# Optimization experiments

Hardware: AMD Instinct MI355X
Metric: run time of the kernel (lower is better)

The kernel has to match this reference:

```python
import jax, jax.numpy as jnp
import numpy as np

N_HEAD = 8
N_EMBD = 768
T_MAX = 1024


def setup_inputs() -> dict:
    key = jax.random.key(0)
    ks = jax.random.split(key, 5)
    B, T, C = 8, 1024, N_EMBD
    x = jax.random.normal(ks[0], (B, T, C), dtype=jnp.float32)
    c_attn_weight = jax.random.normal(ks[1], (3 * C, C), dtype=jnp.float32) * (1.0 / np.sqrt(C))
    c_attn_bias = jax.random.normal(ks[2], (3 * C,), dtype=jnp.float32) * 0.02
    c_proj_weight = jax.random.normal(ks[3], (C, C), dtype=jnp.float32) * (1.0 / np.sqrt(C))
    c_proj_bias = jax.random.normal(ks[4], (C,), dtype=jnp.float32) * 0.02
    bias = jnp.tril(jnp.ones((T_MAX, T_MAX), dtype=jnp.int32))[None, None]  # (1,1,Tmax,Tmax)
    return {
        "x": x,
        "c_attn_weight": c_attn_weight,
        "c_attn_bias": c_attn_bias,
        "c_proj_weight": c_proj_weight,
        "c_proj_bias": c_proj_bias,
        "bias": bias,
    }


def reference(x, c_attn_weight, c_attn_bias, c_proj_weight, c_proj_bias, bias):
    B, T, C = x.shape
    H = N_HEAD
    D = C // H  # head dim
    qkv = jnp.einsum("btc,fc->btf", x, c_attn_weight) + c_attn_bias  # (B,T,3C)
    q, k, v = jnp.split(qkv, 3, axis=-1)
    q = q.reshape(B, T, H, D).transpose(0, 2, 1, 3)  # (B,H,T,D)
    k = k.reshape(B, T, H, D).transpose(0, 2, 1, 3)
    v = v.reshape(B, T, H, D).transpose(0, 2, 1, 3)
    att = jnp.einsum("bhqd,bhkd->bhqk", q, k) * (1.0 / np.sqrt(D))  # (B,H,T,T)
    mask = bias[:, :, :T, :T] == 0
    att = jnp.where(mask, jnp.float32(-jnp.inf), att)
    att = jax.nn.softmax(att, axis=-1)
    y = jnp.einsum("bhqk,bhkd->bhqd", att, v)  # (B,H,T,D)
    y = y.transpose(0, 2, 1, 3).reshape(B, T, C)
    y = jnp.einsum("btc,fc->btf", y, c_proj_weight) + c_proj_bias
    return y
```

## Files before the change

### kernel.cpp

```cpp
#include <hip/hip_runtime.h>
#include <hip/hip_bf16.h>
#include <stdint.h>


typedef unsigned short ushort_t;
typedef __attribute__((ext_vector_type(8))) short short8;
typedef __attribute__((ext_vector_type(4))) float floatx4;
typedef __attribute__((ext_vector_type(4))) unsigned short ushort4v;

#define MFMA16(a, b, c) __builtin_amdgcn_mfma_f32_16x16x32_bf16(a, b, c, 0, 0, 0)
#define NEG_BIG (-1e30f)

__device__ __forceinline__ unsigned short f2bf(float f) {
  union { float f; unsigned int u; } v; v.f = f;
  unsigned int r = (v.u + 0x7FFFu + ((v.u >> 16) & 1u)) >> 16;
  return (unsigned short)r;
}

__device__ __forceinline__ unsigned int packbf2(float a, float b) {
  union { __hip_bfloat162 h; unsigned int u; } cv;
  cv.h = __float22bfloat162_rn(make_float2(a, b));
  return cv.u;
}

#define GLOAD16(src, dst)                                              \
  __builtin_amdgcn_global_load_lds(                                    \
      (const __attribute__((address_space(1))) void*)(src),            \
      (__attribute__((address_space(3))) void*)(dst), 16, 0, 0)

#define WAITBAR(VM)                                                    \
  do {                                                                 \
    asm volatile("s_waitcnt vmcnt(" #VM ")" ::: "memory");             \
    __builtin_amdgcn_s_barrier();                                      \
  } while (0)

#define WAITBAR_LGKM(VM)                                               \
  do {                                                                 \
    asm volatile("s_waitcnt vmcnt(" #VM ") lgkmcnt(0)" ::: "memory");  \
    __builtin_amdgcn_s_barrier();                                      \
  } while (0)

__global__ __launch_bounds__(256) void cvt3(
    const float* __restrict__ x, const float* __restrict__ wa,
    const float* __restrict__ wp, ushort_t* __restrict__ xb,
    ushort_t* __restrict__ wab, ushort_t* __restrict__ wpb)
{
  const int n1 = (8192 * 768) / 4, n2 = (2304 * 768) / 4;
  int i = blockIdx.x * 256 + threadIdx.x;
  const float* in; ushort_t* out;
  if (i < n1)            { in = x;  out = xb; }
  else if (i < n1 + n2)  { in = wa; out = wab; i -= n1; }
  else                   { in = wp; out = wpb; i -= (n1 + n2); }
  float4 v = *(const float4*)(in + (size_t)i * 4);
  ushort4v o;
  o.x = f2bf(v.x); o.y = f2bf(v.y); o.z = f2bf(v.z); o.w = f2bf(v.w);
  *(ushort4v*)(out + (size_t)i * 4) = o;
}

#define GEMM_STAGE(BUF, OFF)                                           \
  do {                                                                 \
    ushort_t* lA = &As[BUF][wid * 512];                                \
    ushort_t* lB = &Bs[BUF][wid * 512];                                \
    const ushort_t* pA = gA + (OFF);                                   \
    const ushort_t* pB = gB + (OFF);                                   \
    GLOAD16(pA, lA);                                                   \
    GLOAD16(pA + (size_t)64 * 768, lA + 64 * 32);                      \
    GLOAD16(pB, lB);                                                   \
    GLOAD16(pB + (size_t)64 * 768, lB + 64 * 32);                      \
  } while (0)

#define GEMM_COMPUTE(BUF)                                              \
  do {                                                                 \
    short8 af[4], bf[4];                                               \
    _Pragma("unroll")                                                  \
    for (int t_ = 0; t_ < 4; ++t_) {                                   \
      af[t_] = *(const short8*)&As[BUF][(wm + t_ * 16 + l15) * 32 + sw]; \
      bf[t_] = *(const short8*)&Bs[BUF][(wn + t_ * 16 + l15) * 32 + sw]; \
    }                                                                  \
    __builtin_amdgcn_s_setprio(1);                                     \
    _Pragma("unroll")                                                  \
    for (int tm = 0; tm < 4; ++tm)                                     \
      _Pragma("unroll")                                                \
      for (int tn = 0; tn < 4; ++tn)                                   \
        acc[tm][tn] = MFMA16(af[tm], bf[tn], acc[tm][tn]);             \
    __builtin_amdgcn_s_setprio(0);                                     \
  } while (0)

#define GEMM_KLOOP                                                     \
  do {                                                                 \
    GEMM_STAGE(0, 0);                                                  \
    GEMM_STAGE(1, 32);                                                 \
    _Pragma("unroll")                                                  \
    for (int t = 0; t < 24; ++t) {                                     \
      if (t < 23) WAITBAR(4); else WAITBAR(0);                         \
      if (t + 2 < 24) GEMM_STAGE((t + 2) % 3, (t + 2) * 32);           \
      GEMM_COMPUTE(t % 3);                                             \
    }                                                                  \
  } while (0)

__global__ __launch_bounds__(256) void gemm_qkv(
    const ushort_t* __restrict__ A,
    const ushort_t* __restrict__ W,
    const float* __restrict__ bias,
    ushort_t* __restrict__ QK,
    ushort_t* __restrict__ VT)
{
  const int K = 768;
  __shared__ ushort_t As[3][128 * 32];
  __shared__ ushort_t Bs[3][128 * 32];

  const int tid  = threadIdx.x;
  const int lane = tid & 63;
  const int l15  = lane & 15;
  const int quad = lane >> 4;
  const int wid  = tid >> 6;
  const int m0 = blockIdx.x * 128;
  const int n0 = blockIdx.y * 128;
  const int wm = (wid >> 1) * 64;
  const int wn = (wid & 1) * 64;
  const int srow = tid >> 2;
  const int scol = (((tid & 3) ^ ((srow ^ (srow >> 2)) & 3))) * 8;
  const int sw = (quad ^ ((l15 ^ (l15 >> 2)) & 3)) * 8;

  floatx4 acc[4][4] = {};

  const ushort_t* gA = A + (size_t)(m0 + srow) * K + scol;
  const ushort_t* gB = W + (size_t)(n0 + srow) * K + scol;

  GEMM_KLOOP;

  const float QSCALE = 0.10206207261596577f * 1.4426950408889634f;

#pragma unroll
  for (int tn = 0; tn < 4; ++tn) {
    const int gc = n0 + wn + tn * 16 + l15;
    const float bv = bias[gc];
    const bool isv = (gc >= 1536);
    const bool isq = (gc < 768);
    const int hh = (gc - 1536) / 96, dd = (gc - 1536) % 96;
#pragma unroll
    for (int tm = 0; tm < 4; ++tm) {
      const int gr = m0 + wm + tm * 16 + quad * 4;
#pragma unroll
      for (int r = 0; r < 4; ++r) {
        float val = acc[tm][tn][r] + bv;
        const int row = gr + r;
        if (!isv) {
          if (isq) val *= QSCALE;
          QK[(size_t)row * 1536 + gc] = f2bf(val);
        } else {
          const int bb = row >> 10, tt = row & 1023;
          const int tt2 = (tt & ~0x1C) | (((tt >> 4) & 1) << 2) |
                          (((tt >> 2) & 3) << 3);
          VT[(((size_t)(bb * 8 + hh)) * 96 + dd) * 1024 + tt2] = f2bf(val);
        }
      }
    }
  }
}

__global__ __launch_bounds__(256) void gemm_proj(
    const ushort_t* __restrict__ A,
    const ushort_t* __restrict__ W,
    const float* __restrict__ bias,
    float* __restrict__ C,
    int M, int N)
{
  const int K = 768;
  __shared__ ushort_t As[3][128 * 32];
  __shared__ ushort_t Bs[3][128 * 32];

  const int tid  = threadIdx.x;
  const int lane = tid & 63;
  const int l15  = lane & 15;
  const int quad = lane >> 4;
  const int wid  = tid >> 6;
  const int m0 = blockIdx.x * 128;
  const int n0 = blockIdx.y * 128;
  const int wm = (wid >> 1) * 64;
  const int wn = (wid & 1) * 64;
  const int srow = tid >> 2;
  const int scol = (((tid & 3) ^ ((srow ^ (srow >> 2)) & 3))) * 8;
  const int sw = (quad ^ ((l15 ^ (l15 >> 2)) & 3)) * 8;

  floatx4 acc[4][4] = {};

  const ushort_t* gA = A + (size_t)(m0 + srow) * K + scol;
  const ushort_t* gB = W + (size_t)(n0 + srow) * K + scol;

  GEMM_KLOOP;

#pragma unroll
  for (int tn = 0; tn < 4; ++tn) {
    const int gc = n0 + wn + tn * 16 + l15;
    const float bv = bias[gc];
#pragma unroll
    for (int tm = 0; tm < 4; ++tm) {
      const int gr = m0 + wm + tm * 16 + quad * 4;
#pragma unroll
      for (int r = 0; r < 4; ++r)
        C[(size_t)(gr + r) * N + gc] = acc[tm][tn][r] + bv;
    }
  }
}

__global__ __launch_bounds__(256) void attn_fused(
    const ushort_t* __restrict__ QK,
    const ushort_t* __restrict__ VT,
    ushort_t* __restrict__ y)
{
  __shared__ ushort_t Ks[2][64 * 96];
  __shared__ ushort_t Vt[2][96 * 72];

  const int tid  = threadIdx.x;
  const int lane = tid & 63;
  const int l15  = lane & 15;
  const int quad = lane >> 4;
  const int wid  = tid >> 6;
  const int bh = blockIdx.y;
  const int b = bh >> 3;
  const int h = bh & 7;
  const int qoff = h * 96;

  const int cA = blockIdx.x;
  const int cB = 31 - cA;
  const int myChunk = (wid < 2) ? cA : cB;
  const int q0w = myChunk * 32 + (wid & 1) * 16;
  const int kend = cB * 32 + 32;
  const int rq = q0w + l15;

  const size_t rowbase = (size_t)b * 1024;
  const ushort_t* vtb = VT + (size_t)bh * 96 * 1024;

  const int ke0 = wid * 1536 + lane * 8;
  const int vd  = (tid >> 3);
  const int vkc = (tid & 7) * 8;

  short8 qf[3];
#pragma unroll
  for (int c = 0; c < 3; ++c)
    qf[c] = *(const short8*)(QK + (rowbase + q0w + l15) * 1536 + qoff +
                             c * 32 + quad * 8);

  float m_i = NEG_BIG;
  float l_i = 0.f;
  floatx4 O[6] = {};

  short8 vreg[3];

#pragma unroll
  for (int g = 0; g < 3; ++g)
    vreg[g] = *(const short8*)(vtb + (size_t)(g * 32 + vd) * 1024 + vkc);
#pragma unroll
  for (int i = 0; i < 3; ++i) {
    const int e = ke0 + i * 512;
    const int kr = e / 96, kc = e % 96;
    GLOAD16(QK + (rowbase + kr) * 1536 + 768 + qoff + kc,
            &Ks[0][wid * 1536 + i * 512]);
  }
#pragma unroll
  for (int g = 0; g < 3; ++g)
    *(short8*)&Vt[0][(g * 32 + vd) * 72 + vkc] = vreg[g];
#pragma unroll
  for (int g = 0; g < 3; ++g)
    vreg[g] = *(const short8*)(vtb + (size_t)(g * 32 + vd) * 1024 + 64 + vkc);

  int cur = 0;
  for (int k0 = 0; k0 < kend; k0 += 64) {
    const int nk = k0 + 64;
    const bool more = (nk < kend);

    if (more) WAITBAR_LGKM(3); else WAITBAR_LGKM(0);

    if (more) {
#pragma unroll
      for (int i = 0; i < 3; ++i) {
        const int e = ke0 + i * 512;
        const int kr = e / 96, kc = e % 96;
        GLOAD16(QK + (rowbase + nk + kr) * 1536 + 768 + qoff + kc,
                &Ks[cur ^ 1][wid * 1536 + i * 512]);
      }
    }

    if (k0 < q0w + 16) {
      floatx4 s[4] = {};
      __builtin_amdgcn_s_setprio(1);
#pragma unroll
      for (int t = 0; t < 4; ++t) {
#pragma unroll
        for (int c = 0; c < 3; ++c) {
          short8 kf = *(const short8*)
              &Ks[cur][(t * 16 + l15) * 96 + c * 32 + quad * 8];
          s[t] = MFMA16(kf, qf[c], s[t]);
        }
      }
      __builtin_amdgcn_s_setprio(0);
      float p[4][4];
      if (k0 + 64 <= q0w) {
#pragma unroll
        for (int t = 0; t < 4; ++t)
#pragma unroll
          for (int j = 0; j < 4; ++j) p[t][j] = s[t][j];
      } else {
        const int kq = k0 + quad * 4;
#pragma unroll
        for (int t = 0; t < 4; ++t)
#pragma unroll
          for (int j = 0; j < 4; ++j)
            p[t][j] = (kq + t * 16 + j <= rq) ? s[t][j] : NEG_BIG;
      }
      float m0v = fmaxf(fmaxf(p[0][0], p[0][1]), fmaxf(p[0][2], p[0][3]));
      float m1v = fmaxf(fmaxf(p[1][0], p[1][1]), fmaxf(p[1][2], p[1][3]));
      float m2v = fmaxf(fmaxf(p[2][0], p[2][1]), fmaxf(p[2][2], p[2][3]));
      float m3v = fmaxf(fmaxf(p[3][0], p[3][1]), fmaxf(p[3][2], p[3][3]));
      float mt = fmaxf(fmaxf(m0v, m1v), fmaxf(m2v, m3v));
      mt = fmaxf(mt, __shfl_xor(mt, 16));
      mt = fmaxf(mt, __shfl_xor(mt, 32));
      if (!__all(mt - m_i <= 8.0f)) {
        const float mn = fmaxf(m_i, mt);
        const float al = __builtin_amdgcn_exp2f(m_i - mn);
        m_i = mn;
        l_i *= al;
#pragma unroll
        for (int j = 0; j < 4; ++j) {
          const float alr = __shfl(al, quad * 4 + j);
#pragma unroll
          for (int f = 0; f < 6; ++f) O[f][j] *= alr;
        }
      }
      float rs = 0.f;
#pragma unroll
      for (int t = 0; t < 4; ++t)
#pragma unroll
        for (int j = 0; j < 4; ++j) {
          p[t][j] = __builtin_amdgcn_exp2f(p[t][j] - m_i);
          rs += p[t][j];
        }
      rs += __shfl_xor(rs, 16);
      rs += __shfl_xor(rs, 32);
      l_i += rs;
      union { short8 s8; unsigned int u[4]; } pf0, pf1;
      pf0.u[0] = packbf2(p[0][0], p[0][1]);
      pf0.u[1] = packbf2(p[0][2], p[0][3]);
      pf0.u[2] = packbf2(p[1][0], p[1][1]);
      pf0.u[3] = packbf2(p[1][2], p[1][3]);
      pf1.u[0] = packbf2(p[2][0], p[2][1]);
      pf1.u[1] = packbf2(p[2][2], p[2][3]);
      pf1.u[2] = packbf2(p[3][0], p[3][1]);
      pf1.u[3] = packbf2(p[3][2], p[3][3]);
      __builtin_amdgcn_s_setprio(1);
#pragma unroll
      for (int f = 0; f < 6; ++f) {
        short8 vf0 = *(const short8*)&Vt[cur][(f * 16 + l15) * 72 + quad * 8];
        O[f] = MFMA16(pf0.s8, vf0, O[f]);
        short8 vf1 = *(const short8*)
            &Vt[cur][(f * 16 + l15) * 72 + 32 + quad * 8];
        O[f] = MFMA16(pf1.s8, vf1, O[f]);
      }
      __builtin_amdgcn_s_setprio(0);
    }

    if (more) {
#pragma unroll
      for (int g = 0; g < 3; ++g)
        *(short8*)&Vt[cur ^ 1][(g * 32 + vd) * 72 + vkc] = vreg[g];
      if (nk + 64 < kend) {
#pragma unroll
        for (int g = 0; g < 3; ++g)
          vreg[g] = *(const short8*)
              (vtb + (size_t)(g * 32 + vd) * 1024 + nk + 64 + vkc);
      }
    }
    cur ^= 1;
  }

  float inv[4];
#pragma unroll
  for (int j = 0; j < 4; ++j) {
    const float lj = __shfl(l_i, quad * 4 + j);
    inv[j] = 1.0f / fmaxf(lj, 1e-20f);
  }
#pragma unroll
  for (int j = 0; j < 4; ++j) {
    const size_t row = rowbase + q0w + quad * 4 + j;
#pragma unroll
    for (int f = 0; f < 6; ++f)
      y[row * 768 + qoff + f * 16 + l15] = f2bf(O[f][j] * inv[j]);
  }
}

extern "C" void kernel_launch(void* const* d_in, const int* in_sizes, int n_in,
                              void* d_out, int out_size, void* d_ws, size_t ws_size,
                              hipStream_t stream)
{
  const float* x_f  = (const float*)d_in[0];
  const float* wa_f = (const float*)d_in[1];
  const float* ba_f = (const float*)d_in[2];
  const float* wp_f = (const float*)d_in[3];
  const float* bp_f = (const float*)d_in[4];
  float* out = (float*)d_out;

  ushort_t* xb  = (ushort_t*)d_ws;
  ushort_t* wab = xb  + (size_t)8192 * 768;
  ushort_t* wpb = wab + (size_t)2304 * 768;
  ushort_t* QK  = wpb + (size_t)768 * 768;
  ushort_t* VT  = QK  + (size_t)8192 * 1536;
  ushort_t* yw  = VT  + (size_t)8192 * 768;

  cvt3<<<8448, 256, 0, stream>>>(x_f, wa_f, wp_f, xb, wab, wpb);

  gemm_qkv<<<dim3(64, 18), 256, 0, stream>>>(xb, wab, ba_f, QK, VT);
  attn_fused<<<dim3(16, 64), 256, 0, stream>>>(QK, VT, yw);
  gemm_proj<<<dim3(64, 6), 256, 0, stream>>>(yw, wpb, bp_f, out,
                                             8192, 768);
}
```

Before: 220.6 us.

## Drop LDS staging; use single-wave blocks loading operands directly from global

Both GEMMs and the attention kernel are rewritten to use single-wavefront blocks that load MFMA operands straight from global memory into registers, with register-level triple buffering in the GEMMs. This removes LDS tiles, barriers and async global-to-LDS copies. Attention drops the paired-chunk load balancing in favour of one 16-row query tile per block. The trade-off is a loss of data reuse across waves, so global/L2 traffic goes up, V reads become strided, and small blocks may load-balance poorly across the causal triangle.

```diff
diff --git a/kernel.cpp b/kernel.cpp
--- a/kernel.cpp
+++ b/kernel.cpp
@@ -22,23 +22,6 @@
   cv.h = __float22bfloat162_rn(make_float2(a, b));
   return cv.u;
 }
-
-#define GLOAD16(src, dst)                                              \
-  __builtin_amdgcn_global_load_lds(                                    \
-      (const __attribute__((address_space(1))) void*)(src),            \
-      (__attribute__((address_space(3))) void*)(dst), 16, 0, 0)
-
-#define WAITBAR(VM)                                                    \
-  do {                                                                 \
-    asm volatile("s_waitcnt vmcnt(" #VM ")" ::: "memory");             \
-    __builtin_amdgcn_s_barrier();                                      \
-  } while (0)
-
-#define WAITBAR_LGKM(VM)                                               \
-  do {                                                                 \
-    asm volatile("s_waitcnt vmcnt(" #VM ") lgkmcnt(0)" ::: "memory");  \
-    __builtin_amdgcn_s_barrier();                                      \
-  } while (0)
 
 __global__ __launch_bounds__(256) void cvt3(
     const float* __restrict__ x, const float* __restrict__ wa,
@@ -57,90 +40,74 @@
   *(ushort4v*)(out + (size_t)i * 4) = o;
 }
 
-#define GEMM_STAGE(BUF, OFF)                                           \
+#define SLD(AA, BB, KO)                                                \
   do {                                                                 \
-    ushort_t* lA = &As[BUF][wid * 512];                                \
-    ushort_t* lB = &Bs[BUF][wid * 512];                                \
-    const ushort_t* pA = gA + (OFF);                                   \
-    const ushort_t* pB = gB + (OFF);                                   \
-    GLOAD16(pA, lA);                                                   \
-    GLOAD16(pA + (size_t)64 * 768, lA + 64 * 32);                      \
-    GLOAD16(pB, lB);                                                   \
-    GLOAD16(pB + (size_t)64 * 768, lB + 64 * 32);                      \
-  } while (0)
-
-#define GEMM_COMPUTE(BUF)                                              \
-  do {                                                                 \
-    short8 af[4], bf[4];                                               \
     _Pragma("unroll")                                                  \
     for (int t_ = 0; t_ < 4; ++t_) {                                   \
-      af[t_] = *(const short8*)&As[BUF][(wm + t_ * 16 + l15) * 32 + sw]; \
-      bf[t_] = *(const short8*)&Bs[BUF][(wn + t_ * 16 + l15) * 32 + sw]; \
+      AA[t_] = *(const short8*)(pA[t_] + (KO));                        \
+      BB[t_] = *(const short8*)(pB[t_] + (KO));                        \
     }                                                                  \
+  } while (0)
+
+#define SCOMP(AA, BB)                                                  \
+  do {                                                                 \
     __builtin_amdgcn_s_setprio(1);                                     \
     _Pragma("unroll")                                                  \
     for (int tm = 0; tm < 4; ++tm)                                     \
       _Pragma("unroll")                                                \
       for (int tn = 0; tn < 4; ++tn)                                   \
-        acc[tm][tn] = MFMA16(af[tm], bf[tn], acc[tm][tn]);             \
+        acc[tm][tn] = MFMA16(AA[tm], BB[tn], acc[tm][tn]);             \
     __builtin_amdgcn_s_setprio(0);                                     \
   } while (0)
 
-#define GEMM_KLOOP                                                     \
-  do {                                                                 \
-    GEMM_STAGE(0, 0);                                                  \
-    GEMM_STAGE(1, 32);                                                 \
-    _Pragma("unroll")                                                  \
-    for (int t = 0; t < 24; ++t) {                                     \
-      if (t < 23) WAITBAR(4); else WAITBAR(0);                         \
-      if (t + 2 < 24) GEMM_STAGE((t + 2) % 3, (t + 2) * 32);           \
-      GEMM_COMPUTE(t % 3);                                             \
-    }                                                                  \
-  } while (0)
-
-__global__ __launch_bounds__(256) void gemm_qkv(
+#define SGEMM_BODY(ABASE, WBASE)                                       \
+  const int tid  = threadIdx.x;                                        \
+  const int l15  = tid & 15;                                           \
+  const int quad = tid >> 4;                                           \
+  const int m0 = blockIdx.x * 64;                                      \
+  const int n0 = blockIdx.y * 64;                                      \
+  floatx4 acc[4][4] = {};                                              \
+  const ushort_t* pA[4];                                               \
+  const ushort_t* pB[4];                                               \
+  _Pragma("unroll")                                                    \
+  for (int t_ = 0; t_ < 4; ++t_) {                                     \
+    pA[t_] = (ABASE) + (size_t)(m0 + t_ * 16 + l15) * 768 + quad * 8;  \
+    pB[t_] = (WBASE) + (size_t)(n0 + t_ * 16 + l15) * 768 + quad * 8;  \
+  }                                                                    \
+  short8 a0[4], b0[4], a1[4], b1[4], a2[4], b2[4];                     \
+  SLD(a0, b0, 0);                                                      \
+  SLD(a1, b1, 32);                                                     \
+  _Pragma("unroll")                                                    \
+  for (int kk = 0; kk < 768; kk += 96) {                               \
+    SLD(a2, b2, kk + 64);                                              \
+    SCOMP(a0, b0);                                                     \
+    if (kk + 96 < 768) SLD(a0, b0, kk + 96);                           \
+    SCOMP(a1, b1);                                                     \
+    if (kk + 128 < 768) SLD(a1, b1, kk + 128);                         \
+    SCOMP(a2, b2);                                                     \
+  }
+
+__global__ __launch_bounds__(64, 2) void gemm_qkv(
     const ushort_t* __restrict__ A,
     const ushort_t* __restrict__ W,
     const float* __restrict__ bias,
     ushort_t* __restrict__ QK,
     ushort_t* __restrict__ VT)
 {
-  const int K = 768;
-  __shared__ ushort_t As[3][128 * 32];
-  __shared__ ushort_t Bs[3][128 * 32];
-
-  const int tid  = threadIdx.x;
-  const int lane = tid & 63;
-  const int l15  = lane & 15;
-  const int quad = lane >> 4;
-  const int wid  = tid >> 6;
-  const int m0 = blockIdx.x * 128;
-  const int n0 = blockIdx.y * 128;
-  const int wm = (wid >> 1) * 64;
-  const int wn = (wid & 1) * 64;
-  const int srow = tid >> 2;
-  const int scol = (((tid & 3) ^ ((srow ^ (srow >> 2)) & 3))) * 8;
-  const int sw = (quad ^ ((l15 ^ (l15 >> 2)) & 3)) * 8;
-
-  floatx4 acc[4][4] = {};
-
-  const ushort_t* gA = A + (size_t)(m0 + srow) * K + scol;
-  const ushort_t* gB = W + (size_t)(n0 + srow) * K + scol;
-
-  GEMM_KLOOP;
+  SGEMM_BODY(A, W);
 
   const float QSCALE = 0.10206207261596577f * 1.4426950408889634f;
 
 #pragma unroll
   for (int tn = 0; tn < 4; ++tn) {
-    const int gc = n0 + wn + tn * 16 + l15;
+    const int gc = n0 + tn * 16 + l15;
     const float bv = bias[gc];
     const bool isv = (gc >= 1536);
     const bool isq = (gc < 768);
     const int hh = (gc - 1536) / 96, dd = (gc - 1536) % 96;
 #pragma unroll
     for (int tm = 0; tm < 4; ++tm) {
-      const int gr = m0 + wm + tm * 16 + quad * 4;
+      const int gr = m0 + tm * 16 + quad * 4;
 #pragma unroll
       for (int r = 0; r < 4; ++r) {
         float val = acc[tm][tn][r] + bv;
@@ -159,44 +126,22 @@
   }
 }
 
-__global__ __launch_bounds__(256) void gemm_proj(
+__global__ __launch_bounds__(64, 2) void gemm_proj(
     const ushort_t* __restrict__ A,
     const ushort_t* __restrict__ W,
     const float* __restrict__ bias,
     float* __restrict__ C,
     int M, int N)
 {
-  const int K = 768;
-  __shared__ ushort_t As[3][128 * 32];
-  __shared__ ushort_t Bs[3][128 * 32];
-
-  const int tid  = threadIdx.x;
-  const int lane = tid & 63;
-  const int l15  = lane & 15;
-  const int quad = lane >> 4;
-  const int wid  = tid >> 6;
-  const int m0 = blockIdx.x * 128;
-  const int n0 = blockIdx.y * 128;
-  const int wm = (wid >> 1) * 64;
-  const int wn = (wid & 1) * 64;
-  const int srow = tid >> 2;
-  const int scol = (((tid & 3) ^ ((srow ^ (srow >> 2)) & 3))) * 8;
-  const int sw = (quad ^ ((l15 ^ (l15 >> 2)) & 3)) * 8;
-
-  floatx4 acc[4][4] = {};
-
-  const ushort_t* gA = A + (size_t)(m0 + srow) * K + scol;
-  const ushort_t* gB = W + (size_t)(n0 + srow) * K + scol;
-
-  GEMM_KLOOP;
+  SGEMM_BODY(A, W);
 
 #pragma unroll
   for (int tn = 0; tn < 4; ++tn) {
-    const int gc = n0 + wn + tn * 16 + l15;
+    const int gc = n0 + tn * 16 + l15;
     const float bv = bias[gc];
 #pragma unroll
     for (int tm = 0; tm < 4; ++tm) {
-      const int gr = m0 + wm + tm * 16 + quad * 4;
+      const int gr = m0 + tm * 16 + quad * 4;
 #pragma unroll
       for (int r = 0; r < 4; ++r)
         C[(size_t)(gr + r) * N + gc] = acc[tm][tn][r] + bv;
@@ -204,37 +149,26 @@
   }
 }
 
-__global__ __launch_bounds__(256) void attn_fused(
+__global__ __launch_bounds__(64, 3) void attn_fused(
     const ushort_t* __restrict__ QK,
     const ushort_t* __restrict__ VT,
     ushort_t* __restrict__ y)
 {
-  __shared__ ushort_t Ks[2][64 * 96];
-  __shared__ ushort_t Vt[2][96 * 72];
-
   const int tid  = threadIdx.x;
-  const int lane = tid & 63;
-  const int l15  = lane & 15;
-  const int quad = lane >> 4;
-  const int wid  = tid >> 6;
+  const int l15  = tid & 15;
+  const int quad = tid >> 4;
   const int bh = blockIdx.y;
   const int b = bh >> 3;
   const int h = bh & 7;
   const int qoff = h * 96;
 
-  const int cA = blockIdx.x;
-  const int cB = 31 - cA;
-  const int myChunk = (wid < 2) ? cA : cB;
-  const int q0w = myChunk * 32 + (wid & 1) * 16;
-  const int kend = cB * 32 + 32;
+  const int q0w = blockIdx.x * 16;
   const int rq = q0w + l15;
+  const int kendw = q0w + 16;
 
   const size_t rowbase = (size_t)b * 1024;
   const ushort_t* vtb = VT + (size_t)bh * 96 * 1024;
-
-  const int ke0 = wid * 1536 + lane * 8;
-  const int vd  = (tid >> 3);
-  const int vkc = (tid & 7) * 8;
+  const ushort_t* kbase = QK + rowbase * 1536 + 768 + qoff;
 
   short8 qf[3];
 #pragma unroll
@@ -246,132 +180,91 @@
   float l_i = 0.f;
   floatx4 O[6] = {};
 
-  short8 vreg[3];
-
-#pragma unroll
-  for (int g = 0; g < 3; ++g)
-    vreg[g] = *(const short8*)(vtb + (size_t)(g * 32 + vd) * 1024 + vkc);
-#pragma unroll
-  for (int i = 0; i < 3; ++i) {
-    const int e = ke0 + i * 512;
-    const int kr = e / 96, kc = e % 96;
-    GLOAD16(QK + (rowbase + kr) * 1536 + 768 + qoff + kc,
-            &Ks[0][wid * 1536 + i * 512]);
-  }
-#pragma unroll
-  for (int g = 0; g < 3; ++g)
-    *(short8*)&Vt[0][(g * 32 + vd) * 72 + vkc] = vreg[g];
-#pragma unroll
-  for (int g = 0; g < 3; ++g)
-    vreg[g] = *(const short8*)(vtb + (size_t)(g * 32 + vd) * 1024 + 64 + vkc);
-
-  int cur = 0;
-  for (int k0 = 0; k0 < kend; k0 += 64) {
-    const int nk = k0 + 64;
-    const bool more = (nk < kend);
-
-    if (more) WAITBAR_LGKM(3); else WAITBAR_LGKM(0);
-
-    if (more) {
-#pragma unroll
-      for (int i = 0; i < 3; ++i) {
-        const int e = ke0 + i * 512;
-        const int kr = e / 96, kc = e % 96;
-        GLOAD16(QK + (rowbase + nk + kr) * 1536 + 768 + qoff + kc,
-                &Ks[cur ^ 1][wid * 1536 + i * 512]);
+  for (int k0 = 0; k0 < kendw; k0 += 64) {
+    floatx4 s[4] = {};
+    short8 kf[4][3];
+#pragma unroll
+    for (int t = 0; t < 4; ++t)
+#pragma unroll
+      for (int c = 0; c < 3; ++c)
+        kf[t][c] = *(const short8*)
+            (kbase + (size_t)(k0 + t * 16 + l15) * 1536 + c * 32 + quad * 8);
+    __builtin_amdgcn_s_setprio(1);
+#pragma unroll
+    for (int t = 0; t < 4; ++t)
+#pragma unroll
+      for (int c = 0; c < 3; ++c)
+        s[t] = MFMA16(kf[t][c], qf[c], s[t]);
+    __builtin_amdgcn_s_setprio(0);
+
+    float p[4][4];
+    if (k0 + 64 <= q0w) {
+#pragma unroll
+      for (int t = 0; t < 4; ++t)
+#pragma unroll
+        for (int j = 0; j < 4; ++j) p[t][j] = s[t][j];
+    } else {
+      const int kq = k0 + quad * 4;
+#pragma unroll
+      for (int t = 0; t < 4; ++t)
+#pragma unroll
+        for (int j = 0; j < 4; ++j)
+          p[t][j] = (kq + t * 16 + j <= rq) ? s[t][j] : NEG_BIG;
+    }
+    float m0v = fmaxf(fmaxf(p[0][0], p[0][1]), fmaxf(p[0][2], p[0][3]));
+    float m1v = fmaxf(fmaxf(p[1][0], p[1][1]), fmaxf(p[1][2], p[1][3]));
+    float m2v = fmaxf(fmaxf(p[2][0], p[2][1]), fmaxf(p[2][2], p[2][3]));
+    float m3v = fmaxf(fmaxf(p[3][0], p[3][1]), fmaxf(p[3][2], p[3][3]));
+    float mt = fmaxf(fmaxf(m0v, m1v), fmaxf(m2v, m3v));
+    mt = fmaxf(mt, __shfl_xor(mt, 16));
+    mt = fmaxf(mt, __shfl_xor(mt, 32));
+    if (!__all(mt - m_i <= 8.0f)) {
+      const float mn = fmaxf(m_i, mt);
+      const float al = __builtin_amdgcn_exp2f(m_i - mn);
+      m_i = mn;
+      l_i *= al;
+#pragma unroll
+      for (int j = 0; j < 4; ++j) {
+        const float alr = __shfl(al, quad * 4 + j);
+#pragma unroll
+        for (int f = 0; f < 6; ++f) O[f][j] *= alr;
       }
     }
-
-    if (k0 < q0w + 16) {
-      floatx4 s[4] = {};
-      __builtin_amdgcn_s_setprio(1);
-#pragma unroll
-      for (int t = 0; t < 4; ++t) {
-#pragma unroll
-        for (int c = 0; c < 3; ++c) {
-          short8 kf = *(const short8*)
-              &Ks[cur][(t * 16 + l15) * 96 + c * 32 + quad * 8];
-          s[t] = MFMA16(kf, qf[c], s[t]);
-        }
+    float rs = 0.f;
+#pragma unroll
+    for (int t = 0; t < 4; ++t)
+#pragma unroll
+      for (int j = 0; j < 4; ++j) {
+        p[t][j] = __builtin_amdgcn_exp2f(p[t][j] - m_i);
+        rs += p[t][j];
       }
-      __builtin_amdgcn_s_setprio(0);
-      float p[4][4];
-      if (k0 + 64 <= q0w) {
-#pragma unroll
-        for (int t = 0; t < 4; ++t)
-#pragma unroll
-          for (int j = 0; j < 4; ++j) p[t][j] = s[t][j];
-      } else {
-        const int kq = k0 + quad * 4;
-#pragma unroll
-        for (int t = 0; t < 4; ++t)
-#pragma unroll
-          for (int j = 0; j < 4; ++j)
-            p[t][j] = (kq + t * 16 + j <= rq) ? s[t][j] : NEG_BIG;
-      }
-      float m0v = fmaxf(fmaxf(p[0][0], p[0][1]), fmaxf(p[0][2], p[0][3]));
-      float m1v = fmaxf(fmaxf(p[1][0], p[1][1]), fmaxf(p[1][2], p[1][3]));
-      float m2v = fmaxf(fmaxf(p[2][0], p[2][1]), fmaxf(p[2][2], p[2][3]));
-      float m3v = fmaxf(fmaxf(p[3][0], p[3][1]), fmaxf(p[3][2], p[3][3]));
-      float mt = fmaxf(fmaxf(m0v, m1v), fmaxf(m2v, m3v));
-      mt = fmaxf(mt, __shfl_xor(mt, 16));
-      mt = fmaxf(mt, __shfl_xor(mt, 32));
-      if (!__all(mt - m_i <= 8.0f)) {
-        const float mn = fmaxf(m_i, mt);
-        const float al = __builtin_amdgcn_exp2f(m_i - mn);
-        m_i = mn;
-        l_i *= al;
-#pragma unroll
-        for (int j = 0; j < 4; ++j) {
-          const float alr = __shfl(al, quad * 4 + j);
-#pragma unroll
-          for (int f = 0; f < 6; ++f) O[f][j] *= alr;
-        }
-      }
-      float rs = 0.f;
-#pragma unroll
-      for (int t = 0; t < 4; ++t)
-#pragma unroll
-        for (int j = 0; j < 4; ++j) {
-          p[t][j] = __builtin_amdgcn_exp2f(p[t][j] - m_i);
-          rs += p[t][j];
-        }
-      rs += __shfl_xor(rs, 16);
-      rs += __shfl_xor(rs, 32);
-      l_i += rs;
-      union { short8 s8; unsigned int u[4]; } pf0, pf1;
-      pf0.u[0] = packbf2(p[0][0], p[0][1]);
-      pf0.u[1] = packbf2(p[0][2], p[0][3]);
-      pf0.u[2] = packbf2(p[1][0], p[1][1]);
-      pf0.u[3] = packbf2(p[1][2], p[1][3]);
-      pf1.u[0] = packbf2(p[2][0], p[2][1]);
-      pf1.u[1] = packbf2(p[2][2], p[2][3]);
-      pf1.u[2] = packbf2(p[3][0], p[3][1]);
-      pf1.u[3] = packbf2(p[3][2], p[3][3]);
-      __builtin_amdgcn_s_setprio(1);
-#pragma unroll
-      for (int f = 0; f < 6; ++f) {
-        short8 vf0 = *(const short8*)&Vt[cur][(f * 16 + l15) * 72 + quad * 8];
-        O[f] = MFMA16(pf0.s8, vf0, O[f]);
-        short8 vf1 = *(const short8*)
-            &Vt[cur][(f * 16 + l15) * 72 + 32 + quad * 8];
-        O[f] = MFMA16(pf1.s8, vf1, O[f]);
-      }
-      __builtin_amdgcn_s_setprio(0);
-    }
-
-    if (more) {
-#pragma unroll
-      for (int g = 0; g < 3; ++g)
-        *(short8*)&Vt[cur ^ 1][(g * 32 + vd) * 72 + vkc] = vreg[g];
-      if (nk + 64 < kend) {
-#pragma unroll
-        for (int g = 0; g < 3; ++g)
-          vreg[g] = *(const short8*)
-              (vtb + (size_t)(g * 32 + vd) * 1024 + nk + 64 + vkc);
-      }
-    }
-    cur ^= 1;
+    rs += __shfl_xor(rs, 16);
+    rs += __shfl_xor(rs, 32);
+    l_i += rs;
+    union { short8 s8; unsigned int u[4]; } pf0, pf1;
+    pf0.u[0] = packbf2(p[0][0], p[0][1]);
+    pf0.u[1] = packbf2(p[0][2], p[0][3]);
+    pf0.u[2] = packbf2(p[1][0], p[1][1]);
+    pf0.u[3] = packbf2(p[1][2], p[1][3]);
+    pf1.u[0] = packbf2(p[2][0], p[2][1]);
+    pf1.u[1] = packbf2(p[2][2], p[2][3]);
+    pf1.u[2] = packbf2(p[3][0], p[3][1]);
+    pf1.u[3] = packbf2(p[3][2], p[3][3]);
+
+    short8 vf[6][2];
+#pragma unroll
+    for (int f = 0; f < 6; ++f)
+#pragma unroll
+      for (int u = 0; u < 2; ++u)
+        vf[f][u] = *(const short8*)
+            (vtb + (size_t)(f * 16 + l15) * 1024 + k0 + u * 32 + quad * 8);
+    __builtin_amdgcn_s_setprio(1);
+#pragma unroll
+    for (int f = 0; f < 6; ++f) {
+      O[f] = MFMA16(pf0.s8, vf[f][0], O[f]);
+      O[f] = MFMA16(pf1.s8, vf[f][1], O[f]);
+    }
+    __builtin_amdgcn_s_setprio(0);
   }
 
   float inv[4];
@@ -409,8 +302,8 @@
 
   cvt3<<<8448, 256, 0, stream>>>(x_f, wa_f, wp_f, xb, wab, wpb);
 
-  gemm_qkv<<<dim3(64, 18), 256, 0, stream>>>(xb, wab, ba_f, QK, VT);
-  attn_fused<<<dim3(16, 64), 256, 0, stream>>>(QK, VT, yw);
-  gemm_proj<<<dim3(64, 6), 256, 0, stream>>>(yw, wpb, bp_f, out,
-                                             8192, 768);
-}
+  gemm_qkv<<<dim3(128, 36), 64, 0, stream>>>(xb, wab, ba_f, QK, VT);
+  attn_fused<<<dim3(64, 64), 64, 0, stream>>>(QK, VT, yw);
+  gemm_proj<<<dim3(128, 12), 64, 0, stream>>>(yw, wpb, bp_f, out,
+                                              8192, 768);
+}
```

Result: slower. 413.6 us (+87.5%).
